# Performance work log

Measured on AMD Instinct MI355X. Metric: run time of the kernel, lower is better.

Reference implementation:

```python
import jax, jax.numpy as jnp
from jax import lax
import numpy as np

B, T, K = 256, 1024, 64


def setup_inputs() -> dict:
    key = jax.random.key(0)
    k1, k2, k3 = jax.random.split(key, 3)
    emissions = jax.random.normal(k1, (B, T, K), dtype=jnp.float32)
    tag_ids = jax.random.randint(k2, (B, T), 0, K, dtype=jnp.int32)
    mask = jnp.ones((B, T), dtype=bool)
    transition_weight = jax.random.normal(k3, (K, K), dtype=jnp.float32)
    return {"emissions": emissions, "tag_ids": tag_ids, "mask": mask,
            "transition_weight": transition_weight}


def _crf_log_likelihood(emissions, tags, mask, trans):
    # emissions: [B,T,K], tags/mask: [B,T], trans: [K,K]
    maskf = mask.astype(emissions.dtype)
    # sequence score: unary emissions at gold tags + pairwise transitions
    unary = jnp.take_along_axis(emissions, tags[..., None], axis=2)[..., 0]  # [B,T]
    unary_score = jnp.sum(unary * maskf, axis=1)
    trans_score = jnp.sum(trans[tags[:, :-1], tags[:, 1:]] * maskf[:, 1:], axis=1)
    seq_score = unary_score + trans_score  # [B]
    # log partition via forward (alpha) recursion over time
    def step(alpha, xs):
        e_t, m_t = xs  # [B,K], [B]
        new = jax.nn.logsumexp(alpha[:, :, None] + trans[None], axis=1) + e_t
        alpha = jnp.where(m_t[:, None], new, alpha)  # carry through padding
        return alpha, None
    alpha0 = emissions[:, 0]
    em_t = jnp.swapaxes(emissions, 0, 1)[1:]  # [T-1,B,K]
    m_t = jnp.swapaxes(mask, 0, 1)[1:]        # [T-1,B]
    alpha, _ = lax.scan(step, alpha0, (em_t, m_t))
    log_z = jax.nn.logsumexp(alpha, axis=1)  # [B]
    return seq_score - log_z


def _crf_decode(emissions, mask, trans):
    # Viterbi: forward max recursion with backpointers, then backtrack.
    num_tags = emissions.shape[-1]
    ident = jnp.arange(num_tags, dtype=jnp.int32)[None, :]  # identity bp for padding

    def fstep(delta, xs):
        e_t, m_t = xs  # [B,K], [B]
        scores = delta[:, :, None] + trans[None]  # [B,K_prev,K_cur]
        bp = jnp.argmax(scores, axis=1).astype(jnp.int32)  # [B,K]
        new = jnp.max(scores, axis=1) + e_t
        delta = jnp.where(m_t[:, None], new, delta)
        bp = jnp.where(m_t[:, None], bp, ident)
        return delta, bp

    delta0 = emissions[:, 0]
    em_t = jnp.swapaxes(emissions, 0, 1)[1:]
    m_t = jnp.swapaxes(mask, 0, 1)[1:]
    delta, bps = lax.scan(fstep, delta0, (em_t, m_t))  # bps: [T-1,B,K]
    last_tag = jnp.argmax(delta, axis=1).astype(jnp.int32)  # [B]

    def bstep(tag, bp_t):
        prev = jnp.take_along_axis(bp_t, tag[:, None], axis=1)[:, 0]
        return prev, tag

    first_tag, tags_rest = lax.scan(bstep, last_tag, bps, reverse=True)
    decoded = jnp.concatenate([first_tag[:, None], jnp.swapaxes(tags_rest, 0, 1)], axis=1)
    return decoded  # [B,T]


def reference(emissions, tag_ids, mask, transition_weight):
    ll = _crf_log_likelihood(emissions, tag_ids, mask, transition_weight)
    loss = -jnp.mean(ll)
    decoded = _crf_decode(emissions, mask, transition_weight)
    mask_i = mask.astype(jnp.int32)
    tag_accuracy = (jnp.sum((decoded == tag_ids).astype(jnp.int32) * mask_i)
                    / jnp.sum(mask_i))
    decoded_masked = decoded * mask_i  # padded positions zeroed (ragged stand-in)
    return loss, decoded_masked, tag_accuracy
```

## Files before the change

### kernel.cpp

```cpp
#include <hip/hip_runtime.h>

#define BB 256
#define TT 1024
#define KK 64
#define CS 65


__device__ __forceinline__ float rlane(float x, int i) {
  return __int_as_float(__builtin_amdgcn_readlane(__float_as_int(x), i));
}
#define RL(S, i) rlane(S, i)

__device__ __forceinline__ float wavemax(float v) {
#pragma unroll
  for (int off = 1; off <= 32; off <<= 1) v = fmaxf(v, __shfl_xor(v, off));
  return v;
}

#define CFQ4(S, a, b, c, d) \
  q0 = __builtin_fmaf(RL(S, a), Ecol[eb + (a)], q0); \
  q1 = __builtin_fmaf(RL(S, b), Ecol[eb + (b)], q1); \
  q2 = __builtin_fmaf(RL(S, c), Ecol[eb + (c)], q2); \
  q3 = __builtin_fmaf(RL(S, d), Ecol[eb + (d)], q3);
#define CFQALL(S) \
  CFQ4(S, 0, 1, 2, 3)     CFQ4(S, 4, 5, 6, 7)     CFQ4(S, 8, 9, 10, 11) \
  CFQ4(S, 12, 13, 14, 15) CFQ4(S, 16, 17, 18, 19) CFQ4(S, 20, 21, 22, 23) \
  CFQ4(S, 24, 25, 26, 27) CFQ4(S, 28, 29, 30, 31) CFQ4(S, 32, 33, 34, 35) \
  CFQ4(S, 36, 37, 38, 39) CFQ4(S, 40, 41, 42, 43) CFQ4(S, 44, 45, 46, 47) \
  CFQ4(S, 48, 49, 50, 51) CFQ4(S, 52, 53, 54, 55) CFQ4(S, 56, 57, 58, 59) \
  CFQ4(S, 60, 61, 62, 63)

#define CFWD_STEP(T_, E_, M_) { \
  int eb = jb65; asm volatile("" : "+v"(eb)); \
  float q0 = 0.f, q1 = 0.f, q2 = 0.f, q3 = 0.f; \
  CFQALL(x) \
  float q = (q0 + q1) + (q2 + q3); \
  q *= (E_); \
  q = (M_) ? q : x; \
  if (((T_) & 7) == 0) { \
    float gm = wavemax(x); \
    q *= __builtin_amdgcn_rcpf(gm); \
    offset += __logf(gm); \
  } \
  x = q; }

#define CVQ(g, a, b, c, d) float vm##g; { \
  float v0 = RL(x, a) + Ccol[cb + (a)]; \
  float v1 = RL(x, b) + Ccol[cb + (b)]; \
  float v2 = RL(x, c) + Ccol[cb + (c)]; \
  float v3 = RL(x, d) + Ccol[cb + (d)]; \
  vm##g = fmaxf(fmaxf(v0, v1), fmaxf(v2, v3)); }

#define CVIT_STEP(T_, E_, M_) { \
  int cb = jb65; asm volatile("" : "+v"(cb)); \
  CVQ(0, 0, 1, 2, 3)      CVQ(1, 4, 5, 6, 7)      CVQ(2, 8, 9, 10, 11) \
  CVQ(3, 12, 13, 14, 15)  CVQ(4, 16, 17, 18, 19)  CVQ(5, 20, 21, 22, 23) \
  CVQ(6, 24, 25, 26, 27)  CVQ(7, 28, 29, 30, 31)  CVQ(8, 32, 33, 34, 35) \
  CVQ(9, 36, 37, 38, 39)  CVQ(10, 40, 41, 42, 43) CVQ(11, 44, 45, 46, 47) \
  CVQ(12, 48, 49, 50, 51) CVQ(13, 52, 53, 54, 55) CVQ(14, 56, 57, 58, 59) \
  CVQ(15, 60, 61, 62, 63) \
  float b0 = fmaxf(vm0, vm1),   b1 = fmaxf(vm2, vm3); \
  float b2 = fmaxf(vm4, vm5),   b3 = fmaxf(vm6, vm7); \
  float b4 = fmaxf(vm8, vm9),   b5 = fmaxf(vm10, vm11); \
  float b6 = fmaxf(vm12, vm13), b7 = fmaxf(vm14, vm15); \
  float best = fmaxf(fmaxf(fmaxf(b0, b1), fmaxf(b2, b3)), \
                     fmaxf(fmaxf(b4, b5), fmaxf(b6, b7))); \
  float nd = (M_) ? (best + (E_)) : x; \
  x = nd; }

#define AG(i0, i1, i2, i3, i4, i5, i6, i7) { \
  float v0 = RL(x2, i0) + Ccol[db + (i0)]; \
  float v1 = RL(x2, i1) + Ccol[db + (i1)]; \
  float v2 = RL(x2, i2) + Ccol[db + (i2)]; \
  float v3 = RL(x2, i3) + Ccol[db + (i3)]; \
  float v4 = RL(x2, i4) + Ccol[db + (i4)]; \
  float v5 = RL(x2, i5) + Ccol[db + (i5)]; \
  float v6 = RL(x2, i6) + Ccol[db + (i6)]; \
  float v7 = RL(x2, i7) + Ccol[db + (i7)]; \
  bool p0 = v1 > v0; float a0 = p0 ? v1 : v0; int n0 = p0 ? (i1) : (i0); \
  bool p1 = v3 > v2; float a1 = p1 ? v3 : v2; int n1 = p1 ? (i3) : (i2); \
  bool p2 = v5 > v4; float a2 = p2 ? v5 : v4; int n2 = p2 ? (i5) : (i4); \
  bool p3 = v7 > v6; float a3 = p3 ? v7 : v6; int n3 = p3 ? (i7) : (i6); \
  bool r0 = a1 > a0; float bb0 = r0 ? a1 : a0; int m0 = r0 ? n1 : n0; \
  bool r1 = a3 > a2; float bb1 = r1 ? a3 : a2; int m1 = r1 ? n3 : n2; \
  bool s0 = bb1 > bb0; float gg = s0 ? bb1 : bb0; int w0 = s0 ? m1 : m0; \
  bool u0 = gg > bv; bv = u0 ? gg : bv; bi = u0 ? w0 : bi; }

#define RLA(a,b,c,d,e,f,g,h) \
  "v_readlane_b32 s36, %[x], " #a "\n\t" \
  "v_readlane_b32 s37, %[x], " #b "\n\t" \
  "v_readlane_b32 s38, %[x], " #c "\n\t" \
  "v_readlane_b32 s39, %[x], " #d "\n\t" \
  "v_readlane_b32 s40, %[x], " #e "\n\t" \
  "v_readlane_b32 s41, %[x], " #f "\n\t" \
  "v_readlane_b32 s42, %[x], " #g "\n\t" \
  "v_readlane_b32 s43, %[x], " #h "\n\t"
#define RLB(a,b,c,d,e,f,g,h) \
  "v_readlane_b32 s44, %[x], " #a "\n\t" \
  "v_readlane_b32 s45, %[x], " #b "\n\t" \
  "v_readlane_b32 s46, %[x], " #c "\n\t" \
  "v_readlane_b32 s47, %[x], " #d "\n\t" \
  "v_readlane_b32 s48, %[x], " #e "\n\t" \
  "v_readlane_b32 s49, %[x], " #f "\n\t" \
  "v_readlane_b32 s50, %[x], " #g "\n\t" \
  "v_readlane_b32 s51, %[x], " #h "\n\t"

#define FMA8F(E0,E1,E2,E3,E4,E5,E6,E7) \
  "v_mul_f32 v20, s36, v" #E0 "\n\t" \
  "v_mul_f32 v21, s37, v" #E1 "\n\t" \
  "v_mul_f32 v22, s38, v" #E2 "\n\t" \
  "v_mul_f32 v23, s39, v" #E3 "\n\t" \
  "v_fmac_f32 v20, s40, v" #E4 "\n\t" \
  "v_fmac_f32 v21, s41, v" #E5 "\n\t" \
  "v_fmac_f32 v22, s42, v" #E6 "\n\t" \
  "v_fmac_f32 v23, s43, v" #E7 "\n\t"
#define FMA8A(E0,E1,E2,E3,E4,E5,E6,E7) \
  "v_fmac_f32 v20, s36, v" #E0 "\n\t" \
  "v_fmac_f32 v21, s37, v" #E1 "\n\t" \
  "v_fmac_f32 v22, s38, v" #E2 "\n\t" \
  "v_fmac_f32 v23, s39, v" #E3 "\n\t" \
  "v_fmac_f32 v20, s40, v" #E4 "\n\t" \
  "v_fmac_f32 v21, s41, v" #E5 "\n\t" \
  "v_fmac_f32 v22, s42, v" #E6 "\n\t" \
  "v_fmac_f32 v23, s43, v" #E7 "\n\t"
#define FMA8B(E0,E1,E2,E3,E4,E5,E6,E7) \
  "v_fmac_f32 v20, s44, v" #E0 "\n\t" \
  "v_fmac_f32 v21, s45, v" #E1 "\n\t" \
  "v_fmac_f32 v22, s46, v" #E2 "\n\t" \
  "v_fmac_f32 v23, s47, v" #E3 "\n\t" \
  "v_fmac_f32 v20, s48, v" #E4 "\n\t" \
  "v_fmac_f32 v21, s49, v" #E5 "\n\t" \
  "v_fmac_f32 v22, s50, v" #E6 "\n\t" \
  "v_fmac_f32 v23, s51, v" #E7 "\n\t"

#define FWD_DOT_P \
  RLA(0,1,2,3,4,5,6,7) \
  RLB(8,9,10,11,12,13,14,15) \
  FMA8F(64,65,66,67,68,69,70,71) \
  RLA(16,17,18,19,20,21,22,23) \
  FMA8B(72,73,74,75,76,77,78,79) \
  RLB(24,25,26,27,28,29,30,31) \
  FMA8A(80,81,82,83,84,85,86,87) \
  RLA(32,33,34,35,36,37,38,39) \
  FMA8B(88,89,90,91,92,93,94,95) \
  RLB(40,41,42,43,44,45,46,47) \
  FMA8A(96,97,98,99,100,101,102,103) \
  RLA(48,49,50,51,52,53,54,55) \
  FMA8B(104,105,106,107,108,109,110,111) \
  RLB(56,57,58,59,60,61,62,63) \
  FMA8A(112,113,114,115,116,117,118,119) \
  FMA8B(120,121,122,123,124,125,126,127)

#define VG4(S0,S1,S2,S3,E0,E1,E2,E3,RED) \
  "v_add_f32 v16, " #S0 ", v" #E0 "\n\t" \
  "v_add_f32 v17, " #S1 ", v" #E1 "\n\t" \
  "v_add_f32 v18, " #S2 ", v" #E2 "\n\t" \
  "v_add_f32 v19, " #S3 ", v" #E3 "\n\t" \
  "v_max3_f32 v16, v16, v17, v18\n\t" \
  RED "\n\t"

#define VIT_DOT_P \
  RLA(0,1,2,3,4,5,6,7) \
  RLB(8,9,10,11,12,13,14,15) \
  VG4(s36,s37,s38,s39,64,65,66,67,"v_max_f32 v20, v16, v19") \
  VG4(s40,s41,s42,s43,68,69,70,71,"v_max3_f32 v20, v20, v16, v19") \
  RLA(16,17,18,19,20,21,22,23) \
  VG4(s44,s45,s46,s47,72,73,74,75,"v_max3_f32 v20, v20, v16, v19") \
  VG4(s48,s49,s50,s51,76,77,78,79,"v_max3_f32 v20, v20, v16, v19") \
  RLB(24,25,26,27,28,29,30,31) \
  VG4(s36,s37,s38,s39,80,81,82,83,"v_max3_f32 v20, v20, v16, v19") \
  VG4(s40,s41,s42,s43,84,85,86,87,"v_max3_f32 v20, v20, v16, v19") \
  RLA(32,33,34,35,36,37,38,39) \
  VG4(s44,s45,s46,s47,88,89,90,91,"v_max3_f32 v20, v20, v16, v19") \
  VG4(s48,s49,s50,s51,92,93,94,95,"v_max3_f32 v20, v20, v16, v19") \
  RLB(40,41,42,43,44,45,46,47) \
  VG4(s36,s37,s38,s39,96,97,98,99,"v_max3_f32 v20, v20, v16, v19") \
  VG4(s40,s41,s42,s43,100,101,102,103,"v_max3_f32 v20, v20, v16, v19") \
  RLA(48,49,50,51,52,53,54,55) \
  VG4(s44,s45,s46,s47,104,105,106,107,"v_max3_f32 v20, v20, v16, v19") \
  VG4(s48,s49,s50,s51,108,109,110,111,"v_max3_f32 v20, v20, v16, v19") \
  RLB(56,57,58,59,60,61,62,63) \
  VG4(s36,s37,s38,s39,112,113,114,115,"v_max3_f32 v20, v20, v16, v19") \
  VG4(s40,s41,s42,s43,116,117,118,119,"v_max3_f32 v20, v20, v16, v19") \
  VG4(s44,s45,s46,s47,120,121,122,123,"v_max3_f32 v20, v20, v16, v19") \
  VG4(s48,s49,s50,s51,124,125,126,127,"v_max3_f32 v20, v20, v16, v19")

#define AGLD(N,OFF) "global_load_dword v" #N ", v13, %[tp] offset:" #OFF "\n\t"
#define AGLE(N,OFF) "global_load_dword v" #N ", v12, %[ep] offset:" #OFF "\n\t"
#define AGLM(N,OFF) "global_load_dword v" #N ", v14, %[mp] offset:" #OFF "\n\t"

#define ELOADS \
  AGLD(64,0) AGLD(65,256) AGLD(66,512) AGLD(67,768) AGLD(68,1024) AGLD(69,1280) \
  AGLD(70,1536) AGLD(71,1792) AGLD(72,2048) AGLD(73,2304) AGLD(74,2560) AGLD(75,2816) \
  AGLD(76,3072) AGLD(77,3328) AGLD(78,3584) AGLD(79,3840) \
  "v_add_u32 v13, 0x1000, v13\n\t" \
  AGLD(80,0) AGLD(81,256) AGLD(82,512) AGLD(83,768) AGLD(84,1024) AGLD(85,1280) \
  AGLD(86,1536) AGLD(87,1792) AGLD(88,2048) AGLD(89,2304) AGLD(90,2560) AGLD(91,2816) \
  AGLD(92,3072) AGLD(93,3328) AGLD(94,3584) AGLD(95,3840) \
  "v_add_u32 v13, 0x1000, v13\n\t" \
  AGLD(96,0) AGLD(97,256) AGLD(98,512) AGLD(99,768) AGLD(100,1024) AGLD(101,1280) \
  AGLD(102,1536) AGLD(103,1792) AGLD(104,2048) AGLD(105,2304) AGLD(106,2560) AGLD(107,2816) \
  AGLD(108,3072) AGLD(109,3328) AGLD(110,3584) AGLD(111,3840) \
  "v_add_u32 v13, 0x1000, v13\n\t" \
  AGLD(112,0) AGLD(113,256) AGLD(114,512) AGLD(115,768) AGLD(116,1024) AGLD(117,1280) \
  AGLD(118,1536) AGLD(119,1792) AGLD(120,2048) AGLD(121,2304) AGLD(122,2560) AGLD(123,2816) \
  AGLD(124,3072) AGLD(125,3328) AGLD(126,3584) AGLD(127,3840)

#define AMUL(N) "v_mul_f32 v" #N ", 0x3fb8aa3b, v" #N "\n\t"
#define AEXI(N) "v_exp_f32 v" #N ", v" #N "\n\t"
#define EEXPALL \
  AMUL(64) AMUL(65) AMUL(66) AMUL(67) AMUL(68) AMUL(69) AMUL(70) AMUL(71) \
  AMUL(72) AMUL(73) AMUL(74) AMUL(75) AMUL(76) AMUL(77) AMUL(78) AMUL(79) \
  AMUL(80) AMUL(81) AMUL(82) AMUL(83) AMUL(84) AMUL(85) AMUL(86) AMUL(87) \
  AMUL(88) AMUL(89) AMUL(90) AMUL(91) AMUL(92) AMUL(93) AMUL(94) AMUL(95) \
  AMUL(96) AMUL(97) AMUL(98) AMUL(99) AMUL(100) AMUL(101) AMUL(102) AMUL(103) \
  AMUL(104) AMUL(105) AMUL(106) AMUL(107) AMUL(108) AMUL(109) AMUL(110) AMUL(111) \
  AMUL(112) AMUL(113) AMUL(114) AMUL(115) AMUL(116) AMUL(117) AMUL(118) AMUL(119) \
  AMUL(120) AMUL(121) AMUL(122) AMUL(123) AMUL(124) AMUL(125) AMUL(126) AMUL(127) \
  AEXI(64) AEXI(65) AEXI(66) AEXI(67) AEXI(68) AEXI(69) AEXI(70) AEXI(71) \
  AEXI(72) AEXI(73) AEXI(74) AEXI(75) AEXI(76) AEXI(77) AEXI(78) AEXI(79) \
  AEXI(80) AEXI(81) AEXI(82) AEXI(83) AEXI(84) AEXI(85) AEXI(86) AEXI(87) \
  AEXI(88) AEXI(89) AEXI(90) AEXI(91) AEXI(92) AEXI(93) AEXI(94) AEXI(95) \
  AEXI(96) AEXI(97) AEXI(98) AEXI(99) AEXI(100) AEXI(101) AEXI(102) AEXI(103) \
  AEXI(104) AEXI(105) AEXI(106) AEXI(107) AEXI(108) AEXI(109) AEXI(110) AEXI(111) \
  AEXI(112) AEXI(113) AEXI(114) AEXI(115) AEXI(116) AEXI(117) AEXI(118) AEXI(119) \
  AEXI(120) AEXI(121) AEXI(122) AEXI(123) AEXI(124) AEXI(125) AEXI(126) AEXI(127)

#define EMIS16 \
  AGLE(40,0) AGLE(41,256) AGLE(42,512) AGLE(43,768) AGLE(44,1024) AGLE(45,1280) \
  AGLE(46,1536) AGLE(47,1792) AGLE(48,2048) AGLE(49,2304) AGLE(50,2560) AGLE(51,2816) \
  AGLE(52,3072) AGLE(53,3328) AGLE(54,3584) AGLE(55,3840)
#define EMIS8 \
  AGLE(40,0) AGLE(41,256) AGLE(42,512) AGLE(43,768) AGLE(44,1024) AGLE(45,1280) \
  AGLE(46,1536) AGLE(47,1792)
#define EMIS16B \
  AGLE(24,0) AGLE(25,256) AGLE(26,512) AGLE(27,768) AGLE(28,1024) AGLE(29,1280) \
  AGLE(30,1536) AGLE(31,1792) AGLE(32,2048) AGLE(33,2304) AGLE(34,2560) AGLE(35,2816) \
  AGLE(36,3072) AGLE(37,3328) AGLE(38,3584) AGLE(39,3840)
#define EMIS8B \
  AGLE(24,0) AGLE(25,256) AGLE(26,512) AGLE(27,768) AGLE(28,1024) AGLE(29,1280) \
  AGLE(30,1536) AGLE(31,1792)
#define MASK16 \
  AGLM(128,0) AGLM(129,4) AGLM(130,8) AGLM(131,12) AGLM(132,16) AGLM(133,20) \
  AGLM(134,24) AGLM(135,28) AGLM(136,32) AGLM(137,36) AGLM(138,40) AGLM(139,44) \
  AGLM(140,48) AGLM(141,52) AGLM(142,56) AGLM(143,60)
#define MASK16B \
  AGLM(144,0) AGLM(145,4) AGLM(146,8) AGLM(147,12) AGLM(148,16) AGLM(149,20) \
  AGLM(150,24) AGLM(151,28) AGLM(152,32) AGLM(153,36) AGLM(154,40) AGLM(155,44) \
  AGLM(156,48) AGLM(157,52) AGLM(158,56) AGLM(159,60)
#define MASK8B \
  AGLM(144,0) AGLM(145,4) AGLM(146,8) AGLM(147,12) AGLM(148,16) AGLM(149,20) \
  AGLM(150,24) AGLM(151,28)

#define MOVMSK \
  "v_mov_b32 v128, v144\n\tv_mov_b32 v129, v145\n\tv_mov_b32 v130, v146\n\t" \
  "v_mov_b32 v131, v147\n\tv_mov_b32 v132, v148\n\tv_mov_b32 v133, v149\n\t" \
  "v_mov_b32 v134, v150\n\tv_mov_b32 v135, v151\n\tv_mov_b32 v136, v152\n\t" \
  "v_mov_b32 v137, v153\n\tv_mov_b32 v138, v154\n\tv_mov_b32 v139, v155\n\t" \
  "v_mov_b32 v140, v156\n\tv_mov_b32 v141, v157\n\tv_mov_b32 v142, v158\n\t" \
  "v_mov_b32 v143, v159\n\t"
#define MOVEMI \
  "v_mov_b32 v40, v24\n\tv_mov_b32 v41, v25\n\tv_mov_b32 v42, v26\n\t" \
  "v_mov_b32 v43, v27\n\tv_mov_b32 v44, v28\n\tv_mov_b32 v45, v29\n\t" \
  "v_mov_b32 v46, v30\n\tv_mov_b32 v47, v31\n\tv_mov_b32 v48, v32\n\t" \
  "v_mov_b32 v49, v33\n\tv_mov_b32 v50, v34\n\tv_mov_b32 v51, v35\n\t" \
  "v_mov_b32 v52, v36\n\tv_mov_b32 v53, v37\n\tv_mov_b32 v54, v38\n\t" \
  "v_mov_b32 v55, v39\n\t"

#define AEM(D,R) "v_mul_f32 v" #D ", 0x3fb8aa3b, v" #R "\n\t"
#define EMEXP16 \
  AEM(24,40) AEM(25,41) AEM(26,42) AEM(27,43) AEM(28,44) AEM(29,45) AEM(30,46) AEM(31,47) \
  AEM(32,48) AEM(33,49) AEM(34,50) AEM(35,51) AEM(36,52) AEM(37,53) AEM(38,54) AEM(39,55) \
  AEXI(24) AEXI(25) AEXI(26) AEXI(27) AEXI(28) AEXI(29) AEXI(30) AEXI(31) \
  AEXI(32) AEXI(33) AEXI(34) AEXI(35) AEXI(36) AEXI(37) AEXI(38) AEXI(39)
#define EMEXP8 \
  AEM(24,40) AEM(25,41) AEM(26,42) AEM(27,43) AEM(28,44) AEM(29,45) AEM(30,46) AEM(31,47) \
  AEXI(24) AEXI(25) AEXI(26) AEXI(27) AEXI(28) AEXI(29) AEXI(30) AEXI(31)

#define AFSTEP_P(MR,EV) \
  "v_cmp_ne_u32 vcc, 0, v" #MR "\n\t" \
  FWD_DOT_P \
  "v_add_f32 v16, v20, v21\n\t" \
  "v_add_f32 v17, v22, v23\n\t" \
  "v_add_f32 v16, v16, v17\n\t" \
  "v_mul_f32 v16, v16, v" #EV "\n\t" \
  "v_cndmask_b32 %[x], %[x], v16, vcc\n\t"

#define RNRM \
  "v_mov_b32 v17, %[x]\n\t" \
  "ds_swizzle_b32 v18, v17 offset:0x041F\n\t" \
  "s_waitcnt lgkmcnt(0)\n\t" \
  "v_max_f32 v17, v17, v18\n\t" \
  "ds_swizzle_b32 v18, v17 offset:0x081F\n\t" \
  "s_waitcnt lgkmcnt(0)\n\t" \
  "v_max_f32 v17, v17, v18\n\t" \
  "ds_swizzle_b32 v18, v17 offset:0x101F\n\t" \
  "s_waitcnt lgkmcnt(0)\n\t" \
  "v_max_f32 v17, v17, v18\n\t" \
  "ds_swizzle_b32 v18, v17 offset:0x201F\n\t" \
  "s_waitcnt lgkmcnt(0)\n\t" \
  "v_max_f32 v17, v17, v18\n\t" \
  "ds_swizzle_b32 v18, v17 offset:0x401F\n\t" \
  "s_waitcnt lgkmcnt(0)\n\t" \
  "v_max_f32 v17, v17, v18\n\t" \
  "v_readlane_b32 s56, v17, 0\n\t" \
  "v_readlane_b32 s57, v17, 32\n\t" \
  "v_mov_b32 v18, s57\n\t" \
  "v_max_f32 v18, s56, v18\n\t" \
  "v_readlane_b32 s56, v18, 0\n\t"

#define AFSTEPR_P(MR,EV) \
  "v_cmp_ne_u32 vcc, 0, v" #MR "\n\t" \
  FWD_DOT_P \
  "v_add_f32 v16, v20, v21\n\t" \
  "v_add_f32 v17, v22, v23\n\t" \
  "v_add_f32 v16, v16, v17\n\t" \
  "v_mul_f32 v16, v16, v" #EV "\n\t" \
  RNRM \
  "v_cndmask_b32 %[x], %[x], v16, vcc\n\t" \
  "v_rcp_f32 v18, s56\n\t" \
  "v_log_f32 v19, s56\n\t" \
  "v_mul_f32 %[x], %[x], v18\n\t" \
  "v_fmac_f32 %[off], 0x3f317218, v19\n\t"

#define AVSTEP_P(MR,EV) \
  "v_cmp_ne_u32 vcc, 0, v" #MR "\n\t" \
  VIT_DOT_P \
  "v_add_f32 v16, v20, v" #EV "\n\t" \
  "v_cndmask_b32 %[x], %[x], v16, vcc\n\t"

#define FSTEPS16 \
  AFSTEPR_P(128,24) AFSTEP_P(129,25) AFSTEP_P(130,26) AFSTEP_P(131,27) \
  AFSTEP_P(132,28)  AFSTEP_P(133,29) AFSTEP_P(134,30) AFSTEP_P(135,31) \
  AFSTEPR_P(136,32) AFSTEP_P(137,33) AFSTEP_P(138,34) AFSTEP_P(139,35) \
  AFSTEP_P(140,36)  AFSTEP_P(141,37) AFSTEP_P(142,38) AFSTEP_P(143,39)
#define VSTEPS16 \
  AVSTEP_P(128,40) AVSTEP_P(129,41) AVSTEP_P(130,42) AVSTEP_P(131,43) \
  AVSTEP_P(132,44) AVSTEP_P(133,45) AVSTEP_P(134,46) AVSTEP_P(135,47) \
  AVSTEP_P(136,48) AVSTEP_P(137,49) AVSTEP_P(138,50) AVSTEP_P(139,51) \
  AVSTEP_P(140,52) AVSTEP_P(141,53) AVSTEP_P(142,54) AVSTEP_P(143,55)

#define CLOBS \
  "v11","v12","v13","v14","v16","v17","v18","v19","v20","v21","v22","v23", \
  "v24","v25","v26","v27","v28","v29","v30","v31","v32","v33","v34","v35", \
  "v36","v37","v38","v39","v40","v41","v42","v43","v44","v45","v46","v47", \
  "v48","v49","v50","v51","v52","v53","v54","v55", \
  "v64","v65","v66","v67","v68","v69","v70","v71","v72","v73","v74","v75", \
  "v76","v77","v78","v79","v80","v81","v82","v83","v84","v85","v86","v87", \
  "v88","v89","v90","v91","v92","v93","v94","v95","v96","v97","v98","v99", \
  "v100","v101","v102","v103","v104","v105","v106","v107","v108","v109", \
  "v110","v111","v112","v113","v114","v115","v116","v117","v118","v119", \
  "v120","v121","v122","v123","v124","v125","v126","v127","v128","v129", \
  "v130","v131","v132","v133","v134","v135","v136","v137","v138","v139", \
  "v140","v141","v142","v143","v144","v145","v146","v147","v148","v149", \
  "v150","v151","v152","v153","v154","v155","v156","v157","v158","v159", \
  "s36","s37","s38","s39","s40","s41","s42","s43","s44","s45","s46","s47", \
  "s48","s49","s50","s51","s55","s56","s57","s58","s59","vcc","scc","memory"

__global__ __launch_bounds__(512)
__attribute__((amdgpu_waves_per_eu(1, 2)))
void crf_mega_kernel(
    const float* __restrict__ em, const int* __restrict__ mask,
    const float* __restrict__ trans, const int* __restrict__ tags,
    float* __restrict__ out_dec, float* ll_sum, int* match, int* maskSum) {

  __shared__ float Ecol[KK * CS];
  __shared__ float Ccol[KK * CS];
  __shared__ __align__(16) float ckw[64][KK];
  __shared__ float fin[KK];
  __shared__ unsigned char mrow[TT];
  __shared__ unsigned char bpl[TT][KK];
  __shared__ unsigned char segm[32][KK];
  __shared__ unsigned char bs[40];
  __shared__ int redm[32];

  const int b = blockIdx.x;
  const int tid = threadIdx.x;
  const int wv = tid >> 6;
  const int j = tid & 63;
  const int jb65 = j * CS;

  const float* emb = em + (size_t)b * TT * KK;
  const int* mb = mask + (size_t)b * TT;
  const int* tgb = tags + (size_t)b * TT;

  for (int t = tid; t < TT; t += 512) mrow[t] = (unsigned char)(mb[t] ? 1 : 0);
  if (wv == 0) {
#pragma unroll 4
    for (int i = 0; i < KK; ++i) Ecol[jb65 + i] = __expf(trans[i * KK + j]);
  } else if (wv == 1) {
#pragma unroll 4
    for (int i = 0; i < KK; ++i) Ccol[jb65 + i] = trans[i * KK + j];
  }
  __syncthreads();

  if (wv == 0) {
    float raw = emb[j];
    float x, offset;
    {
      float m0 = wavemax(raw);
      offset = m0;
      float s = __expf(raw - m0);
      int eb = jb65; asm volatile("" : "+v"(eb));
      float q0 = 0.f, q1 = 0.f, q2 = 0.f, q3 = 0.f;
      CFQALL(s)
      float q = (q0 + q1) + (q2 + q3);
      q *= __expf(emb[KK + j]);
      x = mrow[1] ? q : s;
    }
    for (int t = 2; t <= 7; ++t) {
      float e = __expf(emb[(size_t)t * KK + j]);
      int m = mrow[t];
      CFWD_STEP(t, e, m)
    }
    asm volatile(
      "s_mov_b32 s55, 0\n\t"
      "v_mov_b32 v12, %[vo]\n\t"
      "v_mov_b32 v13, %[jo]\n\t"
      "v_mov_b32 v14, 32\n\t"
      ELOADS
      MASK16
      EMIS16
      "s_waitcnt vmcnt(0)\n\t"
      EEXPALL
      "9:\n\t"
      EMEXP16
      "v_add_u32 v12, 0x1000, v12\n\t"
      EMIS16
      "v_add_u32 v14, 64, v14\n\t"
      MASK16B
      FSTEPS16
      "s_waitcnt vmcnt(0)\n\t"
      MOVMSK
      "s_add_u32 s55, s55, 1\n\t"
      "s_cmp_lt_u32 s55, 62\n\t"
      "s_cbranch_scc1 9b\n\t"
      EMEXP16
      "v_add_u32 v12, 0x1000, v12\n\t"
      EMIS8
      "v_add_u32 v14, 64, v14\n\t"
      MASK8B
      FSTEPS16
      "s_waitcnt vmcnt(0)\n\t"
      EMEXP8
      AFSTEPR_P(144,24) AFSTEP_P(145,25) AFSTEP_P(146,26) AFSTEP_P(147,27)
      AFSTEP_P(148,28)  AFSTEP_P(149,29) AFSTEP_P(150,30) AFSTEP_P(151,31)
      "s_waitcnt vmcnt(0) lgkmcnt(0)\n\t"
      : [x]"+v"(x), [off]"+v"(offset)
      : [ep]"s"(emb), [mp]"s"(mb), [tp]"s"(trans),
        [vo]"v"(2048 + 4 * j), [jo]"v"(4 * j)
      : CLOBS);

    float ssum = x;
#pragma unroll
    for (int off = 1; off <= 32; off <<= 1) ssum += __shfl_xor(ssum, off);
    if (tid == 0) atomicAdd(ll_sum, -(offset + __logf(ssum)));

  } else if (wv == 1) {
    float x = emb[j];
    unsigned ckoff = (unsigned)(unsigned long long)(&ckw[1][j]);
    asm volatile(
      "s_mov_b32 s55, 0\n\t"
      "v_mov_b32 v11, %[ck]\n\t"
      "v_mov_b32 v12, %[vo]\n\t"
      "v_mov_b32 v13, %[jo]\n\t"
      "v_mov_b32 v14, 4\n\t"
      ELOADS
      MASK16
      EMIS16
      "s_waitcnt vmcnt(0)\n\t"
      "8:\n\t"
      "v_add_u32 v12, 0x1000, v12\n\t"
      EMIS16B
      "v_add_u32 v14, 64, v14\n\t"
      MASK16B
      VSTEPS16
      "ds_write_b32 v11, %[x]\n\t"
      "v_add_u32 v11, 0x100, v11\n\t"
      "s_waitcnt vmcnt(0)\n\t"
      MOVEMI
      MOVMSK
      "s_add_u32 s55, s55, 1\n\t"
      "s_cmp_lt_u32 s55, 62\n\t"
      "s_cbranch_scc1 8b\n\t"
      "v_add_u32 v12, 0x1000, v12\n\t"
      EMIS8B
      "v_add_u32 v14, 64, v14\n\t"
      MASK8B
      VSTEPS16
      "ds_write_b32 v11, %[x]\n\t"
      "s_waitcnt vmcnt(0)\n\t"
      AVSTEP_P(144,24) AVSTEP_P(145,25) AVSTEP_P(146,26) AVSTEP_P(147,27)
      AVSTEP_P(148,28) AVSTEP_P(149,29) AVSTEP_P(150,30) AVSTEP_P(151,31)
      "s_waitcnt vmcnt(0) lgkmcnt(0)\n\t"
      : [x]"+v"(x)
      : [ep]"s"(emb), [mp]"s"(mb), [tp]"s"(trans),
        [vo]"v"(256 + 4 * j), [jo]"v"(4 * j), [ck]"v"(ckoff)
      : CLOBS);
    for (int t = TT - 7; t <= TT - 1; ++t) {
      float e = emb[(size_t)t * KK + j];
      int m = mrow[t];
      CVIT_STEP(t, e, m)
    }
    fin[j] = x;

  } else if (wv == 2) {
    float acc = 0.f;
    int cnt = 0;
    for (int t = j; t < TT; t += 64) {
      if (mb[t]) {
        int tg = tgb[t];
        acc += emb[(size_t)t * KK + tg];
        cnt += 1;
        if (t >= 1) acc += trans[tgb[t - 1] * KK + tg];
      }
    }
#pragma unroll
    for (int off = 1; off <= 32; off <<= 1) {
      acc += __shfl_xor(acc, off);
      cnt += __shfl_xor(cnt, off);
    }
    if (j == 0) { atomicAdd(ll_sum, acc); atomicAdd(maskSum, cnt); }
  }

  __syncthreads();

#pragma unroll 1
  for (int kk = 0; kk < 4; ++kk) {
    int s = wv + 8 * kk;
    int tS = 32 * s + 1;
    int tE = (s == 31) ? (TT - 1) : (32 * s + 32);
    float x2 = (s == 0) ? emb[j] : ckw[2 * s][j];
    float e_nx = emb[(size_t)tS * KK + j];
#pragma unroll 1
    for (int t = tS; t <= tE; ++t) {
      float e = e_nx;
      if (t < tE) e_nx = emb[(size_t)(t + 1) * KK + j];
      int db = jb65; asm volatile("" : "+v"(db));
      float bv = -__builtin_inff(); int bi = 0;
      AG(0, 1, 2, 3, 4, 5, 6, 7)        AG(8, 9, 10, 11, 12, 13, 14, 15)
      AG(16, 17, 18, 19, 20, 21, 22, 23) AG(24, 25, 26, 27, 28, 29, 30, 31)
      AG(32, 33, 34, 35, 36, 37, 38, 39) AG(40, 41, 42, 43, 44, 45, 46, 47)
      AG(48, 49, 50, 51, 52, 53, 54, 55) AG(56, 57, 58, 59, 60, 61, 62, 63)
      int m = mrow[t];
      float nd = m ? (bv + e) : x2;
      int bp = m ? bi : j;
      bpl[t][j] = (unsigned char)bp;
      x2 = nd;
    }
  }
  __syncthreads();

  {
    int j0 = tid & 63;
    int sg = tid >> 6;
    int xs[4]; int tS[4], tE[4];
#pragma unroll
    for (int kk = 0; kk < 4; ++kk) {
      int s = sg + 8 * kk;
      xs[kk] = j0;
      tS[kk] = 32 * s + 1;
      tE[kk] = (s == 31) ? (TT - 1) : (32 * s + 32);
    }
    for (int q = 0; q < 32; ++q) {
#pragma unroll
      for (int kk = 0; kk < 4; ++kk) {
        int t = tE[kk] - q;
        if (t >= tS[kk]) xs[kk] = bpl[t][xs[kk]];
      }
    }
#pragma unroll
    for (int kk = 0; kk < 4; ++kk) segm[sg + 8 * kk][j0] = (unsigned char)xs[kk];
  }
  __syncthreads();

  if (tid == 0) {
    float bd = fin[0];
    int lt = 0;
    for (int i = 1; i < KK; ++i) {
      float v2 = fin[i];
      if (v2 > bd) { bd = v2; lt = i; }
    }
    bs[32] = (unsigned char)lt;
    for (int s = 31; s >= 0; --s) bs[s] = segm[s][bs[s + 1]];
  }
  __syncthreads();

  if (tid < 32) {
    int s = tid;
    int x = bs[s + 1];
    int cnt = 0;
    int tEnd = (s == 31) ? (TT - 1) : (32 * s + 32);
    if (s == 31) {
      int m = mrow[TT - 1];
      out_dec[(size_t)b * TT + TT - 1] = (float)(m ? x : 0);
      cnt += (m && x == tgb[TT - 1]);
    }
    for (int t = tEnd; t >= 32 * s + 1; --t) {
      x = bpl[t][x];
      int m2 = mrow[t - 1];
      out_dec[(size_t)b * TT + t - 1] = (float)(m2 ? x : 0);
      cnt += (m2 && x == tgb[t - 1]);
    }
    redm[s] = cnt;
  }
  __syncthreads();
  if (tid == 0) {
    int c = 0;
    for (int s = 0; s < 32; ++s) c += redm[s];
    atomicAdd(match, c);
  }
}

__global__ void finalize_kernel(const float* ll_sum, const int* match,
                                const int* maskSum, float* d_out) {
  d_out[0] = -(*ll_sum) / (float)BB;
  d_out[1 + BB * TT] = (float)(*match) / (float)(*maskSum);
}

extern "C" void kernel_launch(void* const* d_in, const int* in_sizes, int n_in,
                              void* d_out, int out_size, void* d_ws, size_t ws_size,
                              hipStream_t stream) {
  const float* em = (const float*)d_in[0];
  const int* tags = (const int*)d_in[1];
  const int* mask = (const int*)d_in[2];
  const float* trans = (const float*)d_in[3];
  float* out = (float*)d_out;

  float* ll_sum = (float*)d_ws;
  int* match = (int*)((char*)d_ws + 4);
  int* maskSum = (int*)((char*)d_ws + 8);

  hipMemsetAsync(d_ws, 0, 12, stream);
  crf_mega_kernel<<<BB, 512, 0, stream>>>(em, mask, trans, tags, out + 1,
                                          ll_sum, match, maskSum);
  finalize_kernel<<<1, 1, 0, stream>>>(ll_sum, match, maskSum, out);
}
```

Baseline: 601.2 us.

## Broadcast state vector via LDS and use packed FP32 math in recursions

Instead of 64 v_readlane_b32 instructions per step to broadcast the alpha/delta vector into SGPRs, each lane writes its value to a small LDS buffer and then reads the whole vector back with sixteen ds_read_b128. The dot product (forward) and max-plus (Viterbi) then run on v_pk_mul/v_pk_fma/v_pk_add_f32, with a max3 tree for the Viterbi reduction. This removes the serial readlane bottleneck and halves the VALU op count, but adds an LDS round-trip (write, then read with waitcnt) onto the latency-critical recurrence and uses 64 more VGPRs.

```diff
diff --git a/kernel.cpp b/kernel.cpp
--- a/kernel.cpp
+++ b/kernel.cpp
@@ -86,104 +86,123 @@
   bool s0 = bb1 > bb0; float gg = s0 ? bb1 : bb0; int w0 = s0 ? m1 : m0; \
   bool u0 = gg > bv; bv = u0 ? gg : bv; bi = u0 ? w0 : bi; }
 
-#define RLA(a,b,c,d,e,f,g,h) \
-  "v_readlane_b32 s36, %[x], " #a "\n\t" \
-  "v_readlane_b32 s37, %[x], " #b "\n\t" \
-  "v_readlane_b32 s38, %[x], " #c "\n\t" \
-  "v_readlane_b32 s39, %[x], " #d "\n\t" \
-  "v_readlane_b32 s40, %[x], " #e "\n\t" \
-  "v_readlane_b32 s41, %[x], " #f "\n\t" \
-  "v_readlane_b32 s42, %[x], " #g "\n\t" \
-  "v_readlane_b32 s43, %[x], " #h "\n\t"
-#define RLB(a,b,c,d,e,f,g,h) \
-  "v_readlane_b32 s44, %[x], " #a "\n\t" \
-  "v_readlane_b32 s45, %[x], " #b "\n\t" \
-  "v_readlane_b32 s46, %[x], " #c "\n\t" \
-  "v_readlane_b32 s47, %[x], " #d "\n\t" \
-  "v_readlane_b32 s48, %[x], " #e "\n\t" \
-  "v_readlane_b32 s49, %[x], " #f "\n\t" \
-  "v_readlane_b32 s50, %[x], " #g "\n\t" \
-  "v_readlane_b32 s51, %[x], " #h "\n\t"
-
-#define FMA8F(E0,E1,E2,E3,E4,E5,E6,E7) \
-  "v_mul_f32 v20, s36, v" #E0 "\n\t" \
-  "v_mul_f32 v21, s37, v" #E1 "\n\t" \
-  "v_mul_f32 v22, s38, v" #E2 "\n\t" \
-  "v_mul_f32 v23, s39, v" #E3 "\n\t" \
-  "v_fmac_f32 v20, s40, v" #E4 "\n\t" \
-  "v_fmac_f32 v21, s41, v" #E5 "\n\t" \
-  "v_fmac_f32 v22, s42, v" #E6 "\n\t" \
-  "v_fmac_f32 v23, s43, v" #E7 "\n\t"
-#define FMA8A(E0,E1,E2,E3,E4,E5,E6,E7) \
-  "v_fmac_f32 v20, s36, v" #E0 "\n\t" \
-  "v_fmac_f32 v21, s37, v" #E1 "\n\t" \
-  "v_fmac_f32 v22, s38, v" #E2 "\n\t" \
-  "v_fmac_f32 v23, s39, v" #E3 "\n\t" \
-  "v_fmac_f32 v20, s40, v" #E4 "\n\t" \
-  "v_fmac_f32 v21, s41, v" #E5 "\n\t" \
-  "v_fmac_f32 v22, s42, v" #E6 "\n\t" \
-  "v_fmac_f32 v23, s43, v" #E7 "\n\t"
-#define FMA8B(E0,E1,E2,E3,E4,E5,E6,E7) \
-  "v_fmac_f32 v20, s44, v" #E0 "\n\t" \
-  "v_fmac_f32 v21, s45, v" #E1 "\n\t" \
-  "v_fmac_f32 v22, s46, v" #E2 "\n\t" \
-  "v_fmac_f32 v23, s47, v" #E3 "\n\t" \
-  "v_fmac_f32 v20, s48, v" #E4 "\n\t" \
-  "v_fmac_f32 v21, s49, v" #E5 "\n\t" \
-  "v_fmac_f32 v22, s50, v" #E6 "\n\t" \
-  "v_fmac_f32 v23, s51, v" #E7 "\n\t"
-
-#define FWD_DOT_P \
-  RLA(0,1,2,3,4,5,6,7) \
-  RLB(8,9,10,11,12,13,14,15) \
-  FMA8F(64,65,66,67,68,69,70,71) \
-  RLA(16,17,18,19,20,21,22,23) \
-  FMA8B(72,73,74,75,76,77,78,79) \
-  RLB(24,25,26,27,28,29,30,31) \
-  FMA8A(80,81,82,83,84,85,86,87) \
-  RLA(32,33,34,35,36,37,38,39) \
-  FMA8B(88,89,90,91,92,93,94,95) \
-  RLB(40,41,42,43,44,45,46,47) \
-  FMA8A(96,97,98,99,100,101,102,103) \
-  RLA(48,49,50,51,52,53,54,55) \
-  FMA8B(104,105,106,107,108,109,110,111) \
-  RLB(56,57,58,59,60,61,62,63) \
-  FMA8A(112,113,114,115,116,117,118,119) \
-  FMA8B(120,121,122,123,124,125,126,127)
-
-#define VG4(S0,S1,S2,S3,E0,E1,E2,E3,RED) \
-  "v_add_f32 v16, " #S0 ", v" #E0 "\n\t" \
-  "v_add_f32 v17, " #S1 ", v" #E1 "\n\t" \
-  "v_add_f32 v18, " #S2 ", v" #E2 "\n\t" \
-  "v_add_f32 v19, " #S3 ", v" #E3 "\n\t" \
-  "v_max3_f32 v16, v16, v17, v18\n\t" \
-  RED "\n\t"
-
-#define VIT_DOT_P \
-  RLA(0,1,2,3,4,5,6,7) \
-  RLB(8,9,10,11,12,13,14,15) \
-  VG4(s36,s37,s38,s39,64,65,66,67,"v_max_f32 v20, v16, v19") \
-  VG4(s40,s41,s42,s43,68,69,70,71,"v_max3_f32 v20, v20, v16, v19") \
-  RLA(16,17,18,19,20,21,22,23) \
-  VG4(s44,s45,s46,s47,72,73,74,75,"v_max3_f32 v20, v20, v16, v19") \
-  VG4(s48,s49,s50,s51,76,77,78,79,"v_max3_f32 v20, v20, v16, v19") \
-  RLB(24,25,26,27,28,29,30,31) \
-  VG4(s36,s37,s38,s39,80,81,82,83,"v_max3_f32 v20, v20, v16, v19") \
-  VG4(s40,s41,s42,s43,84,85,86,87,"v_max3_f32 v20, v20, v16, v19") \
-  RLA(32,33,34,35,36,37,38,39) \
-  VG4(s44,s45,s46,s47,88,89,90,91,"v_max3_f32 v20, v20, v16, v19") \
-  VG4(s48,s49,s50,s51,92,93,94,95,"v_max3_f32 v20, v20, v16, v19") \
-  RLB(40,41,42,43,44,45,46,47) \
-  VG4(s36,s37,s38,s39,96,97,98,99,"v_max3_f32 v20, v20, v16, v19") \
-  VG4(s40,s41,s42,s43,100,101,102,103,"v_max3_f32 v20, v20, v16, v19") \
-  RLA(48,49,50,51,52,53,54,55) \
-  VG4(s44,s45,s46,s47,104,105,106,107,"v_max3_f32 v20, v20, v16, v19") \
-  VG4(s48,s49,s50,s51,108,109,110,111,"v_max3_f32 v20, v20, v16, v19") \
-  RLB(56,57,58,59,60,61,62,63) \
-  VG4(s36,s37,s38,s39,112,113,114,115,"v_max3_f32 v20, v20, v16, v19") \
-  VG4(s40,s41,s42,s43,116,117,118,119,"v_max3_f32 v20, v20, v16, v19") \
-  VG4(s44,s45,s46,s47,120,121,122,123,"v_max3_f32 v20, v20, v16, v19") \
-  VG4(s48,s49,s50,s51,124,125,126,127,"v_max3_f32 v20, v20, v16, v19")
+#define XBCAST \
+  "ds_write_b32 v15, %[x]\n\t" \
+  "ds_read_b128 v[160:163], v10\n\t" \
+  "ds_read_b128 v[164:167], v10 offset:16\n\t" \
+  "ds_read_b128 v[168:171], v10 offset:32\n\t" \
+  "ds_read_b128 v[172:175], v10 offset:48\n\t" \
+  "ds_read_b128 v[176:179], v10 offset:64\n\t" \
+  "ds_read_b128 v[180:183], v10 offset:80\n\t" \
+  "ds_read_b128 v[184:187], v10 offset:96\n\t" \
+  "ds_read_b128 v[188:191], v10 offset:112\n\t" \
+  "ds_read_b128 v[192:195], v10 offset:128\n\t" \
+  "ds_read_b128 v[196:199], v10 offset:144\n\t" \
+  "ds_read_b128 v[200:203], v10 offset:160\n\t" \
+  "ds_read_b128 v[204:207], v10 offset:176\n\t" \
+  "ds_read_b128 v[208:211], v10 offset:192\n\t" \
+  "ds_read_b128 v[212:215], v10 offset:208\n\t" \
+  "ds_read_b128 v[216:219], v10 offset:224\n\t" \
+  "ds_read_b128 v[220:223], v10 offset:240\n\t"
+
+#define NF_DOT \
+  XBCAST \
+  "s_waitcnt lgkmcnt(12)\n\t" \
+  "v_pk_mul_f32 v[16:17], v[160:161], v[64:65]\n\t" \
+  "v_pk_mul_f32 v[18:19], v[162:163], v[66:67]\n\t" \
+  "v_pk_mul_f32 v[20:21], v[164:165], v[68:69]\n\t" \
+  "v_pk_mul_f32 v[22:23], v[166:167], v[70:71]\n\t" \
+  "v_pk_fma_f32 v[16:17], v[168:169], v[72:73], v[16:17]\n\t" \
+  "v_pk_fma_f32 v[18:19], v[170:171], v[74:75], v[18:19]\n\t" \
+  "v_pk_fma_f32 v[20:21], v[172:173], v[76:77], v[20:21]\n\t" \
+  "v_pk_fma_f32 v[22:23], v[174:175], v[78:79], v[22:23]\n\t" \
+  "s_waitcnt lgkmcnt(8)\n\t" \
+  "v_pk_fma_f32 v[16:17], v[176:177], v[80:81], v[16:17]\n\t" \
+  "v_pk_fma_f32 v[18:19], v[178:179], v[82:83], v[18:19]\n\t" \
+  "v_pk_fma_f32 v[20:21], v[180:181], v[84:85], v[20:21]\n\t" \
+  "v_pk_fma_f32 v[22:23], v[182:183], v[86:87], v[22:23]\n\t" \
+  "v_pk_fma_f32 v[16:17], v[184:185], v[88:89], v[16:17]\n\t" \
+  "v_pk_fma_f32 v[18:19], v[186:187], v[90:91], v[18:19]\n\t" \
+  "v_pk_fma_f32 v[20:21], v[188:189], v[92:93], v[20:21]\n\t" \
+  "v_pk_fma_f32 v[22:23], v[190:191], v[94:95], v[22:23]\n\t" \
+  "s_waitcnt lgkmcnt(4)\n\t" \
+  "v_pk_fma_f32 v[16:17], v[192:193], v[96:97], v[16:17]\n\t" \
+  "v_pk_fma_f32 v[18:19], v[194:195], v[98:99], v[18:19]\n\t" \
+  "v_pk_fma_f32 v[20:21], v[196:197], v[100:101], v[20:21]\n\t" \
+  "v_pk_fma_f32 v[22:23], v[198:199], v[102:103], v[22:23]\n\t" \
+  "v_pk_fma_f32 v[16:17], v[200:201], v[104:105], v[16:17]\n\t" \
+  "v_pk_fma_f32 v[18:19], v[202:203], v[106:107], v[18:19]\n\t" \
+  "v_pk_fma_f32 v[20:21], v[204:205], v[108:109], v[20:21]\n\t" \
+  "v_pk_fma_f32 v[22:23], v[206:207], v[110:111], v[22:23]\n\t" \
+  "s_waitcnt lgkmcnt(0)\n\t" \
+  "v_pk_fma_f32 v[16:17], v[208:209], v[112:113], v[16:17]\n\t" \
+  "v_pk_fma_f32 v[18:19], v[210:211], v[114:115], v[18:19]\n\t" \
+  "v_pk_fma_f32 v[20:21], v[212:213], v[116:117], v[20:21]\n\t" \
+  "v_pk_fma_f32 v[22:23], v[214:215], v[118:119], v[22:23]\n\t" \
+  "v_pk_fma_f32 v[16:17], v[216:217], v[120:121], v[16:17]\n\t" \
+  "v_pk_fma_f32 v[18:19], v[218:219], v[122:123], v[18:19]\n\t" \
+  "v_pk_fma_f32 v[20:21], v[220:221], v[124:125], v[20:21]\n\t" \
+  "v_pk_fma_f32 v[22:23], v[222:223], v[126:127], v[22:23]\n\t" \
+  "v_add_f32 v16, v16, v18\n\t" \
+  "v_add_f32 v20, v20, v22\n\t" \
+  "v_add_f32 v17, v17, v19\n\t" \
+  "v_add_f32 v21, v21, v23\n\t" \
+  "v_add_f32 v16, v16, v20\n\t" \
+  "v_add_f32 v17, v17, v21\n\t" \
+  "v_add_f32 v16, v16, v17\n\t"
+
+#define VM3(d,a,b,c) "v_max3_f32 v" #d ", v" #a ", v" #b ", v" #c "\n\t"
+#define NV_DOT \
+  XBCAST \
+  "s_waitcnt lgkmcnt(12)\n\t" \
+  "v_pk_add_f32 v[160:161], v[160:161], v[64:65]\n\t" \
+  "v_pk_add_f32 v[162:163], v[162:163], v[66:67]\n\t" \
+  "v_pk_add_f32 v[164:165], v[164:165], v[68:69]\n\t" \
+  "v_pk_add_f32 v[166:167], v[166:167], v[70:71]\n\t" \
+  "v_pk_add_f32 v[168:169], v[168:169], v[72:73]\n\t" \
+  "v_pk_add_f32 v[170:171], v[170:171], v[74:75]\n\t" \
+  "v_pk_add_f32 v[172:173], v[172:173], v[76:77]\n\t" \
+  "v_pk_add_f32 v[174:175], v[174:175], v[78:79]\n\t" \
+  "s_waitcnt lgkmcnt(8)\n\t" \
+  "v_pk_add_f32 v[176:177], v[176:177], v[80:81]\n\t" \
+  "v_pk_add_f32 v[178:179], v[178:179], v[82:83]\n\t" \
+  "v_pk_add_f32 v[180:181], v[180:181], v[84:85]\n\t" \
+  "v_pk_add_f32 v[182:183], v[182:183], v[86:87]\n\t" \
+  "v_pk_add_f32 v[184:185], v[184:185], v[88:89]\n\t" \
+  "v_pk_add_f32 v[186:187], v[186:187], v[90:91]\n\t" \
+  "v_pk_add_f32 v[188:189], v[188:189], v[92:93]\n\t" \
+  "v_pk_add_f32 v[190:191], v[190:191], v[94:95]\n\t" \
+  "s_waitcnt lgkmcnt(4)\n\t" \
+  "v_pk_add_f32 v[192:193], v[192:193], v[96:97]\n\t" \
+  "v_pk_add_f32 v[194:195], v[194:195], v[98:99]\n\t" \
+  "v_pk_add_f32 v[196:197], v[196:197], v[100:101]\n\t" \
+  "v_pk_add_f32 v[198:199], v[198:199], v[102:103]\n\t" \
+  "v_pk_add_f32 v[200:201], v[200:201], v[104:105]\n\t" \
+  "v_pk_add_f32 v[202:203], v[202:203], v[106:107]\n\t" \
+  "v_pk_add_f32 v[204:205], v[204:205], v[108:109]\n\t" \
+  "v_pk_add_f32 v[206:207], v[206:207], v[110:111]\n\t" \
+  "s_waitcnt lgkmcnt(0)\n\t" \
+  "v_pk_add_f32 v[208:209], v[208:209], v[112:113]\n\t" \
+  "v_pk_add_f32 v[210:211], v[210:211], v[114:115]\n\t" \
+  "v_pk_add_f32 v[212:213], v[212:213], v[116:117]\n\t" \
+  "v_pk_add_f32 v[214:215], v[214:215], v[118:119]\n\t" \
+  "v_pk_add_f32 v[216:217], v[216:217], v[120:121]\n\t" \
+  "v_pk_add_f32 v[218:219], v[218:219], v[122:123]\n\t" \
+  "v_pk_add_f32 v[220:221], v[220:221], v[124:125]\n\t" \
+  "v_pk_add_f32 v[222:223], v[222:223], v[126:127]\n\t" \
+  VM3(160,160,161,162) VM3(163,163,164,165) VM3(166,166,167,168) \
+  VM3(169,169,170,171) VM3(172,172,173,174) VM3(175,175,176,177) \
+  VM3(178,178,179,180) VM3(181,181,182,183) VM3(184,184,185,186) \
+  VM3(187,187,188,189) VM3(190,190,191,192) VM3(193,193,194,195) \
+  VM3(196,196,197,198) VM3(199,199,200,201) VM3(202,202,203,204) \
+  VM3(205,205,206,207) VM3(208,208,209,210) VM3(211,211,212,213) \
+  VM3(214,214,215,216) VM3(217,217,218,219) VM3(220,220,221,222) \
+  VM3(160,160,163,166) VM3(169,169,172,175) VM3(178,178,181,184) \
+  VM3(187,187,190,193) VM3(196,196,199,202) VM3(205,205,208,211) \
+  VM3(214,214,217,220) \
+  VM3(160,160,169,178) VM3(187,187,196,205) \
+  VM3(160,160,187,214) \
+  "v_max_f32 v160, v160, v223\n\t"
 
 #define AGLD(N,OFF) "global_load_dword v" #N ", v13, %[tp] offset:" #OFF "\n\t"
 #define AGLE(N,OFF) "global_load_dword v" #N ", v12, %[ep] offset:" #OFF "\n\t"
@@ -277,12 +296,9 @@
   AEM(24,40) AEM(25,41) AEM(26,42) AEM(27,43) AEM(28,44) AEM(29,45) AEM(30,46) AEM(31,47) \
   AEXI(24) AEXI(25) AEXI(26) AEXI(27) AEXI(28) AEXI(29) AEXI(30) AEXI(31)
 
-#define AFSTEP_P(MR,EV) \
+#define NFSTEP(MR,EV) \
   "v_cmp_ne_u32 vcc, 0, v" #MR "\n\t" \
-  FWD_DOT_P \
-  "v_add_f32 v16, v20, v21\n\t" \
-  "v_add_f32 v17, v22, v23\n\t" \
-  "v_add_f32 v16, v16, v17\n\t" \
+  NF_DOT \
   "v_mul_f32 v16, v16, v" #EV "\n\t" \
   "v_cndmask_b32 %[x], %[x], v16, vcc\n\t"
 
@@ -309,12 +325,9 @@
   "v_max_f32 v18, s56, v18\n\t" \
   "v_readlane_b32 s56, v18, 0\n\t"
 
-#define AFSTEPR_P(MR,EV) \
+#define NFSTEPR(MR,EV) \
   "v_cmp_ne_u32 vcc, 0, v" #MR "\n\t" \
-  FWD_DOT_P \
-  "v_add_f32 v16, v20, v21\n\t" \
-  "v_add_f32 v17, v22, v23\n\t" \
-  "v_add_f32 v16, v16, v17\n\t" \
+  NF_DOT \
   "v_mul_f32 v16, v16, v" #EV "\n\t" \
   RNRM \
   "v_cndmask_b32 %[x], %[x], v16, vcc\n\t" \
@@ -323,28 +336,28 @@
   "v_mul_f32 %[x], %[x], v18\n\t" \
   "v_fmac_f32 %[off], 0x3f317218, v19\n\t"
 
-#define AVSTEP_P(MR,EV) \
+#define NVSTEP(MR,EV) \
   "v_cmp_ne_u32 vcc, 0, v" #MR "\n\t" \
-  VIT_DOT_P \
-  "v_add_f32 v16, v20, v" #EV "\n\t" \
+  NV_DOT \
+  "v_add_f32 v16, v160, v" #EV "\n\t" \
   "v_cndmask_b32 %[x], %[x], v16, vcc\n\t"
 
 #define FSTEPS16 \
-  AFSTEPR_P(128,24) AFSTEP_P(129,25) AFSTEP_P(130,26) AFSTEP_P(131,27) \
-  AFSTEP_P(132,28)  AFSTEP_P(133,29) AFSTEP_P(134,30) AFSTEP_P(135,31) \
-  AFSTEPR_P(136,32) AFSTEP_P(137,33) AFSTEP_P(138,34) AFSTEP_P(139,35) \
-  AFSTEP_P(140,36)  AFSTEP_P(141,37) AFSTEP_P(142,38) AFSTEP_P(143,39)
+  NFSTEPR(128,24) NFSTEP(129,25) NFSTEP(130,26) NFSTEP(131,27) \
+  NFSTEP(132,28)  NFSTEP(133,29) NFSTEP(134,30) NFSTEP(135,31) \
+  NFSTEPR(136,32) NFSTEP(137,33) NFSTEP(138,34) NFSTEP(139,35) \
+  NFSTEP(140,36)  NFSTEP(141,37) NFSTEP(142,38) NFSTEP(143,39)
 #define VSTEPS16 \
-  AVSTEP_P(128,40) AVSTEP_P(129,41) AVSTEP_P(130,42) AVSTEP_P(131,43) \
-  AVSTEP_P(132,44) AVSTEP_P(133,45) AVSTEP_P(134,46) AVSTEP_P(135,47) \
-  AVSTEP_P(136,48) AVSTEP_P(137,49) AVSTEP_P(138,50) AVSTEP_P(139,51) \
-  AVSTEP_P(140,52) AVSTEP_P(141,53) AVSTEP_P(142,54) AVSTEP_P(143,55)
+  NVSTEP(128,40) NVSTEP(129,41) NVSTEP(130,42) NVSTEP(131,43) \
+  NVSTEP(132,44) NVSTEP(133,45) NVSTEP(134,46) NVSTEP(135,47) \
+  NVSTEP(136,48) NVSTEP(137,49) NVSTEP(138,50) NVSTEP(139,51) \
+  NVSTEP(140,52) NVSTEP(141,53) NVSTEP(142,54) NVSTEP(143,55)
 
 #define CLOBS \
-  "v11","v12","v13","v14","v16","v17","v18","v19","v20","v21","v22","v23", \
-  "v24","v25","v26","v27","v28","v29","v30","v31","v32","v33","v34","v35", \
-  "v36","v37","v38","v39","v40","v41","v42","v43","v44","v45","v46","v47", \
-  "v48","v49","v50","v51","v52","v53","v54","v55", \
+  "v10","v11","v12","v13","v14","v15","v16","v17","v18","v19","v20","v21", \
+  "v22","v23","v24","v25","v26","v27","v28","v29","v30","v31","v32","v33", \
+  "v34","v35","v36","v37","v38","v39","v40","v41","v42","v43","v44","v45", \
+  "v46","v47","v48","v49","v50","v51","v52","v53","v54","v55", \
   "v64","v65","v66","v67","v68","v69","v70","v71","v72","v73","v74","v75", \
   "v76","v77","v78","v79","v80","v81","v82","v83","v84","v85","v86","v87", \
   "v88","v89","v90","v91","v92","v93","v94","v95","v96","v97","v98","v99", \
@@ -354,8 +367,14 @@
   "v130","v131","v132","v133","v134","v135","v136","v137","v138","v139", \
   "v140","v141","v142","v143","v144","v145","v146","v147","v148","v149", \
   "v150","v151","v152","v153","v154","v155","v156","v157","v158","v159", \
-  "s36","s37","s38","s39","s40","s41","s42","s43","s44","s45","s46","s47", \
-  "s48","s49","s50","s51","s55","s56","s57","s58","s59","vcc","scc","memory"
+  "v160","v161","v162","v163","v164","v165","v166","v167","v168","v169", \
+  "v170","v171","v172","v173","v174","v175","v176","v177","v178","v179", \
+  "v180","v181","v182","v183","v184","v185","v186","v187","v188","v189", \
+  "v190","v191","v192","v193","v194","v195","v196","v197","v198","v199", \
+  "v200","v201","v202","v203","v204","v205","v206","v207","v208","v209", \
+  "v210","v211","v212","v213","v214","v215","v216","v217","v218","v219", \
+  "v220","v221","v222","v223", \
+  "s55","s56","s57","vcc","scc","memory"
 
 __global__ __launch_bounds__(512)
 __attribute__((amdgpu_waves_per_eu(1, 2)))
@@ -366,6 +385,8 @@
 
   __shared__ float Ecol[KK * CS];
   __shared__ float Ccol[KK * CS];
+  __shared__ __align__(16) float xbfF[KK];
+  __shared__ __align__(16) float xbfV[KK];
   __shared__ __align__(16) float ckw[64][KK];
   __shared__ float fin[KK];
   __shared__ unsigned char mrow[TT];
@@ -413,11 +434,16 @@
       int m = mrow[t];
       CFWD_STEP(t, e, m)
     }
+    unsigned xr = (unsigned)(unsigned long long)(&xbfF[0]);
+    unsigned xw = xr + 4u * (unsigned)j;
     asm volatile(
       "s_mov_b32 s55, 0\n\t"
+      "v_mov_b32 v10, %[xr]\n\t"
+      "v_mov_b32 v15, %[xw]\n\t"
       "v_mov_b32 v12, %[vo]\n\t"
       "v_mov_b32 v13, %[jo]\n\t"
       "v_mov_b32 v14, 32\n\t"
+      "s_waitcnt lgkmcnt(0)\n\t"
       ELOADS
       MASK16
       EMIS16
@@ -443,12 +469,12 @@
       FSTEPS16
       "s_waitcnt vmcnt(0)\n\t"
       EMEXP8
-      AFSTEPR_P(144,24) AFSTEP_P(145,25) AFSTEP_P(146,26) AFSTEP_P(147,27)
-      AFSTEP_P(148,28)  AFSTEP_P(149,29) AFSTEP_P(150,30) AFSTEP_P(151,31)
+      NFSTEPR(144,24) NFSTEP(145,25) NFSTEP(146,26) NFSTEP(147,27)
+      NFSTEP(148,28)  NFSTEP(149,29) NFSTEP(150,30) NFSTEP(151,31)
       "s_waitcnt vmcnt(0) lgkmcnt(0)\n\t"
       : [x]"+v"(x), [off]"+v"(offset)
       : [ep]"s"(emb), [mp]"s"(mb), [tp]"s"(trans),
-        [vo]"v"(2048 + 4 * j), [jo]"v"(4 * j)
+        [vo]"v"(2048 + 4 * j), [jo]"v"(4 * j), [xr]"v"(xr), [xw]"v"(xw)
       : CLOBS);
 
     float ssum = x;
@@ -459,12 +485,17 @@
   } else if (wv == 1) {
     float x = emb[j];
     unsigned ckoff = (unsigned)(unsigned long long)(&ckw[1][j]);
+    unsigned xr = (unsigned)(unsigned long long)(&xbfV[0]);
+    unsigned xw = xr + 4u * (unsigned)j;
     asm volatile(
       "s_mov_b32 s55, 0\n\t"
+      "v_mov_b32 v10, %[xr]\n\t"
+      "v_mov_b32 v15, %[xw]\n\t"
       "v_mov_b32 v11, %[ck]\n\t"
       "v_mov_b32 v12, %[vo]\n\t"
       "v_mov_b32 v13, %[jo]\n\t"
       "v_mov_b32 v14, 4\n\t"
+      "s_waitcnt lgkmcnt(0)\n\t"
       ELOADS
       MASK16
       EMIS16
@@ -490,12 +521,13 @@
       VSTEPS16
       "ds_write_b32 v11, %[x]\n\t"
       "s_waitcnt vmcnt(0)\n\t"
-      AVSTEP_P(144,24) AVSTEP_P(145,25) AVSTEP_P(146,26) AVSTEP_P(147,27)
-      AVSTEP_P(148,28) AVSTEP_P(149,29) AVSTEP_P(150,30) AVSTEP_P(151,31)
+      NVSTEP(144,24) NVSTEP(145,25) NVSTEP(146,26) NVSTEP(147,27)
+      NVSTEP(148,28) NVSTEP(149,29) NVSTEP(150,30) NVSTEP(151,31)
       "s_waitcnt vmcnt(0) lgkmcnt(0)\n\t"
       : [x]"+v"(x)
       : [ep]"s"(emb), [mp]"s"(mb), [tp]"s"(trans),
-        [vo]"v"(256 + 4 * j), [jo]"v"(4 * j), [ck]"v"(ckoff)
+        [vo]"v"(256 + 4 * j), [jo]"v"(4 * j), [ck]"v"(ckoff),
+        [xr]"v"(xr), [xw]"v"(xw)
       : CLOBS);
     for (int t = TT - 7; t <= TT - 1; ++t) {
       float e = emb[(size_t)t * KK + j];
```

After: 498.5 us. 1.21x faster.
